# Kernel optimization log

Hardware: AMD Instinct MI355X
Metric: run time of the kernel (lower is better)

Reference implementation:

```python
import jax, jax.numpy as jnp
import numpy as np

DIM = 64
KSZ = 3


def _conv2d(x, w, b):
    # x: (N, C, H, W), w: (O, I, 3, 3), 'same' padding
    y = jax.lax.conv_general_dilated(
        x, w, window_strides=(1, 1), padding=[(1, 1), (1, 1)],
        dimension_numbers=("NCHW", "OIHW", "NCHW"))
    return y + b[None, :, None, None]


def setup_inputs() -> dict:
    key = jax.random.key(0)
    k1, k2, k3, k4, k5 = jax.random.split(key, 5)
    b, c, t, h, w = 2, DIM, 5, 128, 128
    x = jax.random.normal(k1, (b, c, t, h, w), dtype=jnp.float32)
    # Conv3d kernels have temporal extent 1 -> equivalent 2D kernels
    w1 = jax.random.normal(k2, (DIM, DIM, 3, 3), dtype=jnp.float32) * 0.05
    b1 = jax.random.normal(k3, (DIM,), dtype=jnp.float32) * 0.05
    w2 = jax.random.normal(k4, (KSZ * KSZ, DIM, 3, 3), dtype=jnp.float32) * 0.05
    b2 = jax.random.normal(k5, (KSZ * KSZ,), dtype=jnp.float32) * 0.05
    return {"x": x, "w1": w1, "b1": b1, "w2": w2, "b2": b2}


def reference(x, w1, b1, w2, b2):
    b, c, t, h, w = x.shape
    k = KSZ
    K = t * k * k
    # Conv3d with (1,3,3) kernel == 2D conv applied per frame
    xf = x.transpose(0, 2, 1, 3, 4).reshape(b * t, c, h, w)  # (bt, c, h, w)
    y = _conv2d(xf, w1, b1)
    y = jnp.where(y >= 0, y, 0.2 * y)  # LeakyReLU(0.2)
    ker = _conv2d(y, w2, b2)  # (bt, k*k, h, w)
    # rearrange 'b (k1 k2) t h w -> b h w (t k1 k2)'
    ker = ker.reshape(b, t, k * k, h, w).transpose(0, 3, 4, 1, 2).reshape(b, h, w, K)
    ker = ker[:, None]  # (b, 1, h, w, K)
    # kernel_normalize over last dim
    ker = ker - jnp.mean(ker, axis=-1, keepdims=True) + 1.0 / K
    # replicate pad + unfold (gather kxk neighborhoods)
    pad = (k - 1) // 2
    xp = jnp.pad(xf, ((0, 0), (0, 0), (pad, pad), (pad, pad)), mode="edge")
    patches = jnp.stack(
        [xp[:, :, i:i + h, j:j + w] for i in range(k) for j in range(k)],
        axis=-1)  # (bt, c, h, w, k*k) in (k1,k2) order like F.unfold
    # '(b t) (c k1 k2) (h w) -> b c h w (t k1 k2)'
    patches = patches.reshape(b, t, c, h, w, k * k).transpose(0, 2, 3, 4, 1, 5)
    patches = patches.reshape(b, c, h, w, K)
    return jnp.sum(patches * ker, axis=-1)  # (b, c, h, w)
```

## Files before the change

### kernel.cpp

```cpp
#include <hip/hip_runtime.h>
#include <hip/hip_bf16.h>

#define HH 128
#define WW 128
#define CC 64
#define TT 5
#define HW (HH*WW)
#define NI 10

typedef __attribute__((ext_vector_type(8))) short short8;
typedef __attribute__((ext_vector_type(4))) float f32x4;

__device__ __forceinline__ float bf2f(unsigned int bits16) {
  union { unsigned int u; float f; } v; v.u = bits16 << 16; return v.f;
}
__device__ __forceinline__ unsigned short f2bf(float f) {
  __hip_bfloat16 h = __float2bfloat16(f);
  return *reinterpret_cast<unsigned short*>(&h);
}

__global__ __launch_bounds__(256) void pack_w_k(const float* __restrict__ w1,
    const float* __restrict__ w2, unsigned short* __restrict__ wb1,
    unsigned short* __restrict__ wb2) {
  int idx = blockIdx.x*256 + threadIdx.x;
  if (idx < 64*576) {
    int oc = idx / 576, rem = idx - oc*576, kk = rem >> 6, ic = rem & 63;
    wb1[idx] = f2bf(w1[(oc*64 + ic)*9 + kk]);
  }
  if (idx < 16*576) {
    int oc = idx / 576, rem = idx - oc*576, kk = rem >> 6, ic = rem & 63;
    wb2[idx] = (oc < 9) ? f2bf(w2[(oc*64 + ic)*9 + kk]) : (unsigned short)0;
  }
}

__global__ __launch_bounds__(256) void pack_x_k(const float* __restrict__ x,
    unsigned short* __restrict__ xb) {
  __shared__ unsigned short tb[128*72];
  const int tid = threadIdx.x;
  const int n = blockIdx.x >> 7, h = blockIdx.x & 127;
  const int bi = n / 5, ti = n - bi*5;
  const float* xp = x + ((size_t)bi*CC*TT + ti)*HW + (size_t)h*WW;
  for (int e = tid; e < 64*128; e += 256) {
    int ci = e >> 7, w = e & 127;
    tb[w*72 + ci] = f2bf(xp[(size_t)ci*TT*HW + w]);
  }
  __syncthreads();
  unsigned short* dst = xb + ((size_t)n*HW + (size_t)h*WW)*64;
  for (int e = tid; e < 1024; e += 256) {
    int w = e >> 3, c0 = (e & 7) << 3;
    uint4 v = *(const uint4*)(&tb[w*72 + c0]);
    *(uint4*)(&dst[w*64 + c0]) = v;
  }
}

__global__ __launch_bounds__(256) void conv1_mfma(
    const unsigned short* __restrict__ xb, const unsigned short* __restrict__ wb1,
    const float* __restrict__ b1, unsigned short* __restrict__ yb) {
  __shared__ unsigned short xt[324*64];
  const int tid = threadIdx.x;
  const int wave = tid >> 6, lane = tid & 63, q = lane >> 4, r = lane & 15;
  const int n = blockIdx.z, h0 = blockIdx.y << 4, w0 = blockIdx.x << 4;
  const unsigned short* xn = xb + (size_t)n*HW*64;

  for (int e = tid; e < 2592; e += 256) {
    int sp = e >> 3, c = e & 7;
    int sr = sp / 18, sc = sp - sr*18;
    int gh = h0 + sr - 1, gw = w0 + sc - 1;
    uint4 v = make_uint4(0u,0u,0u,0u);
    if (gh >= 0 && gh < HH && gw >= 0 && gw < WW)
      v = *(const uint4*)(xn + ((size_t)(gh*WW + gw))*64 + (c << 3));
    *(uint4*)(&xt[sp*64 + ((c ^ (sp & 7)) << 3)]) = v;
  }
  __syncthreads();

  f32x4 zero4 = {0.f, 0.f, 0.f, 0.f};
  f32x4 acc[4][4];
  #pragma unroll
  for (int i = 0; i < 4; ++i)
    #pragma unroll
    for (int g = 0; g < 4; ++g) acc[i][g] = zero4;

  #pragma unroll
  for (int kk = 0; kk < 9; ++kk) {
    const int dy = kk / 3, dx = kk - dy*3;
    #pragma unroll
    for (int half = 0; half < 2; ++half) {
      short8 a[4];
      #pragma unroll
      for (int g = 0; g < 4; ++g)
        a[g] = *(const short8*)(wb1 + (g*16 + r)*576 + kk*64 + half*32 + (q << 3));
      #pragma unroll
      for (int i = 0; i < 4; ++i) {
        int sp = (wave*4 + i + dy)*18 + (r + dx);
        short8 b = *(const short8*)(&xt[sp*64 + ((((half << 2) | q) ^ (sp & 7)) << 3)]);
        #pragma unroll
        for (int g = 0; g < 4; ++g)
          acc[i][g] = __builtin_amdgcn_mfma_f32_16x16x32_bf16(a[g], b, acc[i][g], 0, 0, 0);
      }
    }
  }

  #pragma unroll
  for (int i = 0; i < 4; ++i) {
    int py = wave*4 + i;
    unsigned short* yp = yb + ((size_t)n*HW + (h0+py)*WW + (w0+r))*64;
    #pragma unroll
    for (int g = 0; g < 4; ++g) {
      int oc0 = g*16 + (q << 2);
      f32x4 bias = *(const f32x4*)(b1 + oc0);
      unsigned int p0, p1;
      float v0 = acc[i][g][0] + bias[0]; v0 = (v0 >= 0.f) ? v0 : 0.2f*v0;
      float v1 = acc[i][g][1] + bias[1]; v1 = (v1 >= 0.f) ? v1 : 0.2f*v1;
      float v2 = acc[i][g][2] + bias[2]; v2 = (v2 >= 0.f) ? v2 : 0.2f*v2;
      float v3 = acc[i][g][3] + bias[3]; v3 = (v3 >= 0.f) ? v3 : 0.2f*v3;
      p0 = (unsigned int)f2bf(v0) | ((unsigned int)f2bf(v1) << 16);
      p1 = (unsigned int)f2bf(v2) | ((unsigned int)f2bf(v3) << 16);
      uint2 pk; pk.x = p0; pk.y = p1;
      *(uint2*)(yp + oc0) = pk;
    }
  }
}

__global__ __launch_bounds__(256) void conv2_mfma(
    const unsigned short* __restrict__ yb, const unsigned short* __restrict__ wb2,
    const float* __restrict__ b2, float* __restrict__ ker0) {
  __shared__ unsigned short yt[324*64];
  const int tid = threadIdx.x;
  const int wave = tid >> 6, lane = tid & 63, q = lane >> 4, r = lane & 15;
  const int n = blockIdx.z, h0 = blockIdx.y << 4, w0 = blockIdx.x << 4;
  const unsigned short* yn = yb + (size_t)n*HW*64;

  for (int e = tid; e < 2592; e += 256) {
    int sp = e >> 3, c = e & 7;
    int sr = sp / 18, sc = sp - sr*18;
    int gh = h0 + sr - 1, gw = w0 + sc - 1;
    uint4 v = make_uint4(0u,0u,0u,0u);
    if (gh >= 0 && gh < HH && gw >= 0 && gw < WW)
      v = *(const uint4*)(yn + ((size_t)(gh*WW + gw))*64 + (c << 3));
    *(uint4*)(&yt[sp*64 + ((c ^ (sp & 7)) << 3)]) = v;
  }
  __syncthreads();

  f32x4 zero4 = {0.f, 0.f, 0.f, 0.f};
  f32x4 acc[4];
  #pragma unroll
  for (int i = 0; i < 4; ++i) acc[i] = zero4;

  #pragma unroll
  for (int kk = 0; kk < 9; ++kk) {
    const int dy = kk / 3, dx = kk - dy*3;
    #pragma unroll
    for (int half = 0; half < 2; ++half) {
      short8 a = *(const short8*)(wb2 + r*576 + kk*64 + half*32 + (q << 3));
      #pragma unroll
      for (int i = 0; i < 4; ++i) {
        int sp = (wave*4 + i + dy)*18 + (r + dx);
        short8 b = *(const short8*)(&yt[sp*64 + ((((half << 2) | q) ^ (sp & 7)) << 3)]);
        acc[i] = __builtin_amdgcn_mfma_f32_16x16x32_bf16(a, b, acc[i], 0, 0, 0);
      }
    }
  }

  #pragma unroll
  for (int i = 0; i < 4; ++i) {
    int py = wave*4 + i;
    #pragma unroll
    for (int t2 = 0; t2 < 4; ++t2) {
      int oc = (q << 2) + t2;
      if (oc < 9)
        ker0[((size_t)n*9 + oc)*HW + (h0+py)*WW + w0 + r] = acc[i][t2] + b2[oc];
    }
  }
}

__global__ __launch_bounds__(256) void dynf_k(
    const unsigned short* __restrict__ xb, const float* __restrict__ ker0,
    float* __restrict__ out) {
  __shared__ float xs[TT*324*4];
  const int tw = threadIdx.x, th = threadIdx.y;
  const int tid = th*16 + tw;
  const int wz = blockIdx.z;
  const int bi = wz >> 2, cq = wz & 3;
  const int h0 = blockIdx.y << 4, w0 = blockIdx.x << 4;
  const int pix = (h0+th)*WW + w0 + tw;

  float kv[45]; float s = 0.f;
  #pragma unroll
  for (int t5 = 0; t5 < TT; ++t5)
    #pragma unroll
    for (int kk = 0; kk < 9; ++kk) {
      float v = ker0[((size_t)(bi*TT + t5)*9 + kk)*HW + pix];
      kv[t5*9 + kk] = v; s += v;
    }
  const float m = (s - 1.f) * (1.f/45.f);
  #pragma unroll
  for (int qq = 0; qq < 45; ++qq) kv[qq] -= m;

  for (int ch = 0; ch < 4; ++ch) {
    const int ci0 = cq*16 + ch*4;
    __syncthreads();
    for (int e = tid; e < TT*324; e += 256) {
      int t5 = e / 324, sp = e - t5*324;
      int rr = sp / 18, cc = sp - rr*18;
      int gh = min(max(h0 + rr - 1, 0), HH-1);
      int gw = min(max(w0 + cc - 1, 0), WW-1);
      uint2 raw = *(const uint2*)(xb + ((size_t)(bi*TT + t5)*HW + gh*WW + gw)*64 + ci0);
      f32x4 f;
      f[0] = bf2f(raw.x & 0xffffu);
      f[1] = bf2f(raw.x >> 16);
      f[2] = bf2f(raw.y & 0xffffu);
      f[3] = bf2f(raw.y >> 16);
      *(f32x4*)(&xs[e << 2]) = f;
    }
    __syncthreads();
    float a0 = 0.f, a1 = 0.f, a2 = 0.f, a3 = 0.f;
    #pragma unroll
    for (int t5 = 0; t5 < TT; ++t5)
      #pragma unroll
      for (int dy = 0; dy < 3; ++dy)
        #pragma unroll
        for (int dx = 0; dx < 3; ++dx) {
          f32x4 xv = *(const f32x4*)(&xs[(t5*324 + (th+dy)*18 + (tw+dx)) << 2]);
          float k = kv[t5*9 + dy*3 + dx];
          a0 = fmaf(xv[0], k, a0); a1 = fmaf(xv[1], k, a1);
          a2 = fmaf(xv[2], k, a2); a3 = fmaf(xv[3], k, a3);
        }
    float* op = out + ((size_t)(bi*CC + ci0))*HW + pix;
    op[0] = a0; op[HW] = a1; op[2*(size_t)HW] = a2; op[3*(size_t)HW] = a3;
  }
}

extern "C" void kernel_launch(void* const* d_in, const int* in_sizes, int n_in,
                              void* d_out, int out_size, void* d_ws, size_t ws_size,
                              hipStream_t stream) {
  const float* x  = (const float*)d_in[0];
  const float* w1 = (const float*)d_in[1];
  const float* b1 = (const float*)d_in[2];
  const float* w2 = (const float*)d_in[3];
  const float* b2 = (const float*)d_in[4];
  float* out = (float*)d_out;

  unsigned short* xb  = (unsigned short*)d_ws;
  unsigned short* yb  = xb + (size_t)NI*HW*64;
  float*          ker0 = (float*)(yb + (size_t)NI*HW*64);
  unsigned short* wb1 = (unsigned short*)(ker0 + (size_t)NI*9*HW);
  unsigned short* wb2 = wb1 + 64*576;

  pack_w_k <<<144, 256, 0, stream>>>(w1, w2, wb1, wb2);
  pack_x_k <<<NI*HH, 256, 0, stream>>>(x, xb);
  conv1_mfma<<<dim3(8,8,NI), 256, 0, stream>>>(xb, wb1, b1, yb);
  conv2_mfma<<<dim3(8,8,NI), 256, 0, stream>>>(yb, wb2, b2, ker0);
  dynf_k   <<<dim3(8,8,8), dim3(16,16), 0, stream>>>(xb, ker0, out);
}
```

Before: 166.9 us.

## Split conv tiles into smaller blocks and halve dynamic-filter channel groups

The two convolutions now use 128-thread blocks covering 8x16 pixels, and conv1 is further split into two 32-channel output groups, so each launch has several times more blocks to fill the GPU. The dynamic-filter kernel now handles 8 channels per block with a single staged load into two shared planes, replacing a four-pass loop with repeated syncs, and its grid doubles. pack_x_k uses a narrower shared-memory pad and 8-byte stores. Smaller tiles raise the halo-load overhead per output pixel and re-read the input across the two conv1 channel groups, in exchange for better occupancy and fewer barriers.

```diff
diff --git a/kernel.cpp b/kernel.cpp
--- a/kernel.cpp
+++ b/kernel.cpp
@@ -35,34 +35,34 @@
 
 __global__ __launch_bounds__(256) void pack_x_k(const float* __restrict__ x,
     unsigned short* __restrict__ xb) {
-  __shared__ unsigned short tb[128*72];
+  __shared__ unsigned short tb[128*68];
   const int tid = threadIdx.x;
   const int n = blockIdx.x >> 7, h = blockIdx.x & 127;
   const int bi = n / 5, ti = n - bi*5;
   const float* xp = x + ((size_t)bi*CC*TT + ti)*HW + (size_t)h*WW;
   for (int e = tid; e < 64*128; e += 256) {
     int ci = e >> 7, w = e & 127;
-    tb[w*72 + ci] = f2bf(xp[(size_t)ci*TT*HW + w]);
+    tb[w*68 + ci] = f2bf(xp[(size_t)ci*TT*HW + w]);
   }
   __syncthreads();
   unsigned short* dst = xb + ((size_t)n*HW + (size_t)h*WW)*64;
-  for (int e = tid; e < 1024; e += 256) {
-    int w = e >> 3, c0 = (e & 7) << 3;
-    uint4 v = *(const uint4*)(&tb[w*72 + c0]);
-    *(uint4*)(&dst[w*64 + c0]) = v;
-  }
-}
-
-__global__ __launch_bounds__(256) void conv1_mfma(
+  for (int e = tid; e < 2048; e += 256) {
+    int w = e >> 4, c = e & 15;
+    *(uint2*)(dst + w*64 + c*4) = *(const uint2*)(&tb[w*68 + c*4]);
+  }
+}
+
+__global__ __launch_bounds__(128, 3) void conv1_mfma(
     const unsigned short* __restrict__ xb, const unsigned short* __restrict__ wb1,
     const float* __restrict__ b1, unsigned short* __restrict__ yb) {
-  __shared__ unsigned short xt[324*64];
+  __shared__ unsigned short xt[180*64];
   const int tid = threadIdx.x;
   const int wave = tid >> 6, lane = tid & 63, q = lane >> 4, r = lane & 15;
-  const int n = blockIdx.z, h0 = blockIdx.y << 4, w0 = blockIdx.x << 4;
+  const int n = blockIdx.z >> 1, ocg = (blockIdx.z & 1) << 5;
+  const int h0 = blockIdx.y << 3, w0 = blockIdx.x << 4;
   const unsigned short* xn = xb + (size_t)n*HW*64;
 
-  for (int e = tid; e < 2592; e += 256) {
+  for (int e = tid; e < 1440; e += 128) {
     int sp = e >> 3, c = e & 7;
     int sr = sp / 18, sc = sp - sr*18;
     int gh = h0 + sr - 1, gw = w0 + sc - 1;
@@ -74,28 +74,25 @@
   __syncthreads();
 
   f32x4 zero4 = {0.f, 0.f, 0.f, 0.f};
-  f32x4 acc[4][4];
+  f32x4 acc[4][2];
   #pragma unroll
   for (int i = 0; i < 4; ++i)
     #pragma unroll
-    for (int g = 0; g < 4; ++g) acc[i][g] = zero4;
+    for (int g = 0; g < 2; ++g) acc[i][g] = zero4;
 
   #pragma unroll
   for (int kk = 0; kk < 9; ++kk) {
     const int dy = kk / 3, dx = kk - dy*3;
     #pragma unroll
     for (int half = 0; half < 2; ++half) {
-      short8 a[4];
-      #pragma unroll
-      for (int g = 0; g < 4; ++g)
-        a[g] = *(const short8*)(wb1 + (g*16 + r)*576 + kk*64 + half*32 + (q << 3));
+      short8 a0 = *(const short8*)(wb1 + (size_t)(ocg +      r)*576 + kk*64 + half*32 + (q << 3));
+      short8 a1 = *(const short8*)(wb1 + (size_t)(ocg + 16 + r)*576 + kk*64 + half*32 + (q << 3));
       #pragma unroll
       for (int i = 0; i < 4; ++i) {
         int sp = (wave*4 + i + dy)*18 + (r + dx);
         short8 b = *(const short8*)(&xt[sp*64 + ((((half << 2) | q) ^ (sp & 7)) << 3)]);
-        #pragma unroll
-        for (int g = 0; g < 4; ++g)
-          acc[i][g] = __builtin_amdgcn_mfma_f32_16x16x32_bf16(a[g], b, acc[i][g], 0, 0, 0);
+        acc[i][0] = __builtin_amdgcn_mfma_f32_16x16x32_bf16(a0, b, acc[i][0], 0, 0, 0);
+        acc[i][1] = __builtin_amdgcn_mfma_f32_16x16x32_bf16(a1, b, acc[i][1], 0, 0, 0);
       }
     }
   }
@@ -105,32 +102,32 @@
     int py = wave*4 + i;
     unsigned short* yp = yb + ((size_t)n*HW + (h0+py)*WW + (w0+r))*64;
     #pragma unroll
-    for (int g = 0; g < 4; ++g) {
-      int oc0 = g*16 + (q << 2);
+    for (int g = 0; g < 2; ++g) {
+      int oc0 = ocg + g*16 + (q << 2);
       f32x4 bias = *(const f32x4*)(b1 + oc0);
-      unsigned int p0, p1;
       float v0 = acc[i][g][0] + bias[0]; v0 = (v0 >= 0.f) ? v0 : 0.2f*v0;
       float v1 = acc[i][g][1] + bias[1]; v1 = (v1 >= 0.f) ? v1 : 0.2f*v1;
       float v2 = acc[i][g][2] + bias[2]; v2 = (v2 >= 0.f) ? v2 : 0.2f*v2;
       float v3 = acc[i][g][3] + bias[3]; v3 = (v3 >= 0.f) ? v3 : 0.2f*v3;
-      p0 = (unsigned int)f2bf(v0) | ((unsigned int)f2bf(v1) << 16);
-      p1 = (unsigned int)f2bf(v2) | ((unsigned int)f2bf(v3) << 16);
-      uint2 pk; pk.x = p0; pk.y = p1;
+      uint2 pk;
+      pk.x = (unsigned int)f2bf(v0) | ((unsigned int)f2bf(v1) << 16);
+      pk.y = (unsigned int)f2bf(v2) | ((unsigned int)f2bf(v3) << 16);
       *(uint2*)(yp + oc0) = pk;
     }
   }
 }
 
-__global__ __launch_bounds__(256) void conv2_mfma(
+__global__ __launch_bounds__(128, 3) void conv2_mfma(
     const unsigned short* __restrict__ yb, const unsigned short* __restrict__ wb2,
     const float* __restrict__ b2, float* __restrict__ ker0) {
-  __shared__ unsigned short yt[324*64];
+  __shared__ unsigned short yt[180*64];
   const int tid = threadIdx.x;
   const int wave = tid >> 6, lane = tid & 63, q = lane >> 4, r = lane & 15;
-  const int n = blockIdx.z, h0 = blockIdx.y << 4, w0 = blockIdx.x << 4;
+  const int n = blockIdx.z;
+  const int h0 = blockIdx.y << 3, w0 = blockIdx.x << 4;
   const unsigned short* yn = yb + (size_t)n*HW*64;
 
-  for (int e = tid; e < 2592; e += 256) {
+  for (int e = tid; e < 1440; e += 128) {
     int sp = e >> 3, c = e & 7;
     int sr = sp / 18, sc = sp - sr*18;
     int gh = h0 + sr - 1, gw = w0 + sc - 1;
@@ -173,14 +170,15 @@
   }
 }
 
-__global__ __launch_bounds__(256) void dynf_k(
+__global__ __launch_bounds__(256, 3) void dynf_k(
     const unsigned short* __restrict__ xb, const float* __restrict__ ker0,
     float* __restrict__ out) {
-  __shared__ float xs[TT*324*4];
+  __shared__ float xs0[TT*324*4];
+  __shared__ float xs1[TT*324*4];
   const int tw = threadIdx.x, th = threadIdx.y;
   const int tid = th*16 + tw;
   const int wz = blockIdx.z;
-  const int bi = wz >> 2, cq = wz & 3;
+  const int bi = wz >> 3, ci0 = (wz & 7) << 3;
   const int h0 = blockIdx.y << 4, w0 = blockIdx.x << 4;
   const int pix = (h0+th)*WW + w0 + tw;
 
@@ -196,23 +194,26 @@
   #pragma unroll
   for (int qq = 0; qq < 45; ++qq) kv[qq] -= m;
 
-  for (int ch = 0; ch < 4; ++ch) {
-    const int ci0 = cq*16 + ch*4;
-    __syncthreads();
-    for (int e = tid; e < TT*324; e += 256) {
-      int t5 = e / 324, sp = e - t5*324;
-      int rr = sp / 18, cc = sp - rr*18;
-      int gh = min(max(h0 + rr - 1, 0), HH-1);
-      int gw = min(max(w0 + cc - 1, 0), WW-1);
-      uint2 raw = *(const uint2*)(xb + ((size_t)(bi*TT + t5)*HW + gh*WW + gw)*64 + ci0);
-      f32x4 f;
-      f[0] = bf2f(raw.x & 0xffffu);
-      f[1] = bf2f(raw.x >> 16);
-      f[2] = bf2f(raw.y & 0xffffu);
-      f[3] = bf2f(raw.y >> 16);
-      *(f32x4*)(&xs[e << 2]) = f;
-    }
-    __syncthreads();
+  for (int e = tid; e < TT*324; e += 256) {
+    int t5 = e / 324, sp = e - t5*324;
+    int rr = sp / 18, cc = sp - rr*18;
+    int gh = min(max(h0 + rr - 1, 0), HH-1);
+    int gw = min(max(w0 + cc - 1, 0), WW-1);
+    uint4 raw = *(const uint4*)(xb + ((size_t)(bi*TT + t5)*HW + gh*WW + gw)*64 + ci0);
+    xs0[(e << 2) + 0] = bf2f(raw.x & 0xffffu);
+    xs0[(e << 2) + 1] = bf2f(raw.x >> 16);
+    xs0[(e << 2) + 2] = bf2f(raw.y & 0xffffu);
+    xs0[(e << 2) + 3] = bf2f(raw.y >> 16);
+    xs1[(e << 2) + 0] = bf2f(raw.z & 0xffffu);
+    xs1[(e << 2) + 1] = bf2f(raw.z >> 16);
+    xs1[(e << 2) + 2] = bf2f(raw.w & 0xffffu);
+    xs1[(e << 2) + 3] = bf2f(raw.w >> 16);
+  }
+  __syncthreads();
+
+  #pragma unroll
+  for (int p = 0; p < 2; ++p) {
+    const float* plane = p ? xs1 : xs0;
     float a0 = 0.f, a1 = 0.f, a2 = 0.f, a3 = 0.f;
     #pragma unroll
     for (int t5 = 0; t5 < TT; ++t5)
@@ -220,12 +221,12 @@
       for (int dy = 0; dy < 3; ++dy)
         #pragma unroll
         for (int dx = 0; dx < 3; ++dx) {
-          f32x4 xv = *(const f32x4*)(&xs[(t5*324 + (th+dy)*18 + (tw+dx)) << 2]);
+          f32x4 xv = *(const f32x4*)(&plane[(t5*324 + (th+dy)*18 + (tw+dx)) << 2]);
           float k = kv[t5*9 + dy*3 + dx];
           a0 = fmaf(xv[0], k, a0); a1 = fmaf(xv[1], k, a1);
           a2 = fmaf(xv[2], k, a2); a3 = fmaf(xv[3], k, a3);
         }
-    float* op = out + ((size_t)(bi*CC + ci0))*HW + pix;
+    float* op = out + ((size_t)(bi*CC + ci0 + p*4))*HW + pix;
     op[0] = a0; op[HW] = a1; op[2*(size_t)HW] = a2; op[3*(size_t)HW] = a3;
   }
 }
@@ -246,9 +247,9 @@
   unsigned short* wb1 = (unsigned short*)(ker0 + (size_t)NI*9*HW);
   unsigned short* wb2 = wb1 + 64*576;
 
-  pack_w_k <<<144, 256, 0, stream>>>(w1, w2, wb1, wb2);
-  pack_x_k <<<NI*HH, 256, 0, stream>>>(x, xb);
-  conv1_mfma<<<dim3(8,8,NI), 256, 0, stream>>>(xb, wb1, b1, yb);
-  conv2_mfma<<<dim3(8,8,NI), 256, 0, stream>>>(yb, wb2, b2, ker0);
-  dynf_k   <<<dim3(8,8,8), dim3(16,16), 0, stream>>>(xb, ker0, out);
-}
+  pack_w_k  <<<144, 256, 0, stream>>>(w1, w2, wb1, wb2);
+  pack_x_k  <<<NI*HH, 256, 0, stream>>>(x, xb);
+  conv1_mfma<<<dim3(8,16,2*NI), 128, 0, stream>>>(xb, wb1, b1, yb);
+  conv2_mfma<<<dim3(8,16,NI), 128, 0, stream>>>(yb, wb2, b2, ker0);
+  dynf_k    <<<dim3(8,8,16), dim3(16,16), 0, stream>>>(xb, ker0, out);
+}
```

Result: faster. 156.7 us (-6.1%).
